# Kernel optimization log

Hardware: AMD Instinct MI355X
Metric: run time of the kernel (lower is better)

## Reference

```python
import jax, jax.numpy as jnp
import numpy as np

EPS = 1e-5

def _layernorm(x, g, b):
    # normalize over last (channel) axis
    mu = jnp.mean(x, axis=-1, keepdims=True)
    var = jnp.var(x, axis=-1, keepdims=True)
    return (x - mu) * jax.lax.rsqrt(var + EPS) * g + b

def _dynamix(xt, wnd, bnd, wnn, bnn):
    # xt: [B, M, N, C]; mixes over the N axis (vectorized form of the per-slice loop)
    B, M, N, C = xt.shape
    d = wnd.shape[1]
    p = xt @ wnd + bnd                       # [B,M,N,d]
    p = p.reshape(B, M, N * d) @ wnn + bnn   # [B,M,N*N]
    p = jax.nn.softmax(p.reshape(B, M, N, N), axis=-1)
    return jnp.einsum('bmij,bmjc->bmic', p, xt)  # [B,M,N,C]

def setup_inputs() -> dict:
    key = jax.random.key(0)
    ks = jax.random.split(key, 10)
    B, C, H, W, d, E = 32, 128, 56, 56, 10, 4
    def n(k, shape, scale=0.02):
        return jax.random.normal(k, shape, jnp.float32) * scale
    return {
        'x': jax.random.normal(ks[0], (B, C, H, W), jnp.float32),
        'ln1_g': jnp.ones((C,), jnp.float32), 'ln1_b': jnp.zeros((C,), jnp.float32),
        'h_wnd': n(ks[1], (C, d)), 'h_bnd': jnp.zeros((d,), jnp.float32),
        'h_wnn': n(ks[2], (W * d, W * W)), 'h_bnn': jnp.zeros((W * W,), jnp.float32),
        'w_wnd': n(ks[3], (C, d)), 'w_bnd': jnp.zeros((d,), jnp.float32),
        'w_wnn': n(ks[4], (H * d, H * H)), 'w_bnn': jnp.zeros((H * H,), jnp.float32),
        'pc_w': n(ks[5], (C, C)), 'pc_b': jnp.zeros((C,), jnp.float32),
        'po_w': n(ks[6], (C, C)), 'po_b': jnp.zeros((C,), jnp.float32),
        'ln2_g': jnp.ones((C,), jnp.float32), 'ln2_b': jnp.zeros((C,), jnp.float32),
        'fc1_w': n(ks[7], (C, E * C)), 'fc1_b': jnp.zeros((E * C,), jnp.float32),
        'fc2_w': n(ks[8], (E * C, C)), 'fc2_b': jnp.zeros((C,), jnp.float32),
    }

def reference(x, ln1_g, ln1_b, h_wnd, h_bnd, h_wnn, h_bnn,
              w_wnd, w_bnd, w_wnn, w_bnn, pc_w, pc_b, po_w, po_b,
              ln2_g, ln2_b, fc1_w, fc1_b, fc2_w, fc2_b):
    # x: [B,C,H,W] -> work channels-last [B,H,W,C]
    xt = jnp.transpose(x, (0, 2, 3, 1))
    # ---- block p1: LN + DynaMixer ----
    u = _layernorm(xt, ln1_g, ln1_b)                 # [B,H,W,C]
    y_h = _dynamix(u, h_wnd, h_bnd, h_wnn, h_bnn)    # mix over W per row
    u_w = jnp.transpose(u, (0, 2, 1, 3))             # [B,W,H,C]
    y_w = _dynamix(u_w, w_wnd, w_bnd, w_wnn, w_bnn)  # mix over H per col
    y_w = jnp.transpose(y_w, (0, 2, 1, 3))           # back to [B,H,W,C]
    y_c = u @ pc_w + pc_b                            # 1x1 conv proj_c
    y = (y_h + y_w + y_c) @ po_w + po_b              # 1x1 conv proj_o
    xt = xt + y                                      # residual (drop_path=0)
    # ---- block p2: LN + MLP ----
    v = _layernorm(xt, ln2_g, ln2_b)
    h = jax.nn.gelu(v @ fc1_w + fc1_b, approximate=False)
    h = h @ fc2_w + fc2_b
    xt = xt + h
    return jnp.transpose(xt, (0, 3, 1, 2))           # [B,C,H,W]
```

## Files before the change

### kernel.cpp

```cpp
#include <hip/hip_runtime.h>
#include <hip/hip_bf16.h>
#include <math.h>

#define BB 32
#define CC 128
#define HH 56
#define WW 56
#define HWHW 3136
#define TOK 100352
#define BH 1792
#define NDP 576
#define NNP 3200

typedef __attribute__((ext_vector_type(8))) short bhalf8;
typedef __attribute__((ext_vector_type(4))) float f32x4;
typedef __attribute__((ext_vector_type(4))) unsigned int u32x4;

__device__ inline unsigned short f2bf(float f) {
  __bf16 h = (__bf16)f;
  unsigned short u;
  __builtin_memcpy(&u, &h, 2);
  return u;
}
__device__ inline float bf2f(unsigned short u) {
  return __uint_as_float(((unsigned int)u) << 16);
}
__device__ inline unsigned int pack2(float a, float b) {
  return (unsigned int)f2bf(a) | ((unsigned int)f2bf(b) << 16);
}
__device__ inline f32x4 MFMA(bhalf8 a, bhalf8 b, f32x4 c) {
  return __builtin_amdgcn_mfma_f32_16x16x32_bf16(a, b, c, 0, 0, 0);
}
template <int CH>
__device__ inline bhalf8 ldsFrag(const unsigned short* base, int row, int chunk) {
  return *reinterpret_cast<const bhalf8*>(base + row * (CH * 8) + ((chunk ^ (row & 7)) * 8));
}
__device__ inline bhalf8 gFrag(const unsigned short* p) {
  return *reinterpret_cast<const bhalf8*>(p);
}
__device__ inline float gelu_f(float x) {
  float x3 = x * x * x;
  float z2 = 1.5957691216057308f * (x + 0.044715f * x3);
  float e = __expf(z2);
  return x * e * __builtin_amdgcn_rcpf(e + 1.0f);
}

__global__ __launch_bounds__(256) void wtrans_kernel(
    const float* __restrict__ hwnn, const float* __restrict__ wwnn,
    const float* __restrict__ pcw, const float* __restrict__ pow_,
    const float* __restrict__ fc1w, const float* __restrict__ fc2w,
    const float* __restrict__ hwnd, const float* __restrict__ wwnd,
    unsigned short* __restrict__ wnnTh, unsigned short* __restrict__ wnnTw,
    unsigned short* __restrict__ pcT, unsigned short* __restrict__ poT,
    unsigned short* __restrict__ fc1T, unsigned short* __restrict__ fc2T,
    unsigned short* __restrict__ wcatT, u32x4* __restrict__ pdzero) {
  __shared__ unsigned short t[64][65];
  int bid = blockIdx.x;
  int tid = threadIdx.x;
  if (bid >= 940) {
    int gt = (bid - 940) * 256 + tid, gs = 64 * 256;
    for (int i = gt; i < 258048; i += gs) { u32x4 z = {0, 0, 0, 0}; pdzero[i] = z; }
    for (int i = gt; i < 128 * 32; i += gs) {
      int k = i >> 5, n = i & 31;
      float v = n < 10 ? hwnd[k * 10 + n] : (n < 20 ? wwnd[k * 10 + (n - 10)] : 0.f);
      wcatT[n * 128 + k] = f2bf(v);
    }
    return;
  }
  const float* src; unsigned short* dst;
  int K, N, Kp, Np, bx, by;
  if (bid < 450)      { src = hwnn; dst = wnnTh; K = 560; N = 3136; Kp = 576; Np = 3200; int b = bid;       bx = b % 50; by = b / 50; }
  else if (bid < 900) { src = wwnn; dst = wnnTw; K = 560; N = 3136; Kp = 576; Np = 3200; int b = bid - 450; bx = b % 50; by = b / 50; }
  else if (bid < 904) { src = pcw;  dst = pcT;   K = 128; N = 128;  Kp = 128; Np = 128;  int b = bid - 900; bx = b % 2;  by = b / 2; }
  else if (bid < 908) { src = pow_; dst = poT;   K = 128; N = 128;  Kp = 128; Np = 128;  int b = bid - 904; bx = b % 2;  by = b / 2; }
  else if (bid < 924) { src = fc1w; dst = fc1T;  K = 128; N = 512;  Kp = 128; Np = 512;  int b = bid - 908; bx = b % 8;  by = b / 8; }
  else                { src = fc2w; dst = fc2T;  K = 512; N = 128;  Kp = 512; Np = 128;  int b = bid - 924; bx = b % 2;  by = b / 2; }
  int n0 = bx * 64, k0 = by * 64;
  for (int idx = tid; idx < 4096; idx += 256) {
    int kk = idx >> 6, nn = idx & 63;
    float v = (k0 + kk < K && n0 + nn < N) ? src[(size_t)(k0 + kk) * N + n0 + nn] : 0.f;
    t[nn][kk] = f2bf(v);
  }
  __syncthreads();
  for (int idx = tid; idx < 4096; idx += 256) {
    int nn = idx >> 6, kk = idx & 63;
    if (n0 + nn < Np && k0 + kk < Kp)
      dst[(size_t)(n0 + nn) * Kp + k0 + kk] = t[nn][kk];
  }
}

__global__ __launch_bounds__(256) void ln1_kernel(const float* __restrict__ x,
    const float* __restrict__ g, const float* __restrict__ bt,
    unsigned short* __restrict__ ubf, unsigned short* __restrict__ xcl) {
  int bh = blockIdx.x;
  int b = bh / HH, h = bh % HH;
  __shared__ float lds[WW][CC + 1];
  __shared__ float mu[WW], rs[WW];
  const float* xp = x + ((size_t)b * CC) * HWHW + (size_t)h * WW;
  for (int idx = threadIdx.x; idx < CC * WW; idx += 256) {
    int c = idx / WW, w = idx % WW;
    lds[w][c] = xp[(size_t)c * HWHW + w];
  }
  __syncthreads();
  if (threadIdx.x < WW) {
    int w = threadIdx.x;
    float s = 0.f, ss = 0.f;
    for (int c = 0; c < CC; ++c) { float v = lds[w][c]; s += v; ss += v * v; }
    float m = s * (1.0f / CC);
    float var = ss * (1.0f / CC) - m * m;
    mu[w] = m; rs[w] = rsqrtf(var + 1e-5f);
  }
  __syncthreads();
  unsigned short* up = ubf + (size_t)bh * (WW * CC);
  unsigned short* xc = xcl + (size_t)bh * (WW * CC);
  for (int idx = threadIdx.x; idx < WW * CC; idx += 256) {
    int w = idx >> 7, c = idx & 127;
    float v = lds[w][c];
    up[idx] = f2bf((v - mu[w]) * rs[w] * g[c] + bt[c]);
    xc[idx] = f2bf(v);
  }
}

__global__ __launch_bounds__(256) void pd_mfma(const unsigned short* __restrict__ ubf,
    const unsigned short* __restrict__ wcatT, const float* __restrict__ hbnd,
    const float* __restrict__ wbnd, unsigned short* __restrict__ pdh,
    unsigned short* __restrict__ pdw) {
  __shared__ __align__(16) unsigned short sU[64 * 128];
  __shared__ __align__(16) unsigned short sW[32 * 128];
  int tid = threadIdx.x;
  int tok0 = blockIdx.x * 64;
  #pragma unroll
  for (int i = 0; i < 4; ++i) {
    int s = i * 256 + tid; int r = s >> 4, c = s & 15;
    u32x4 v = *reinterpret_cast<const u32x4*>(ubf + (size_t)(tok0 + r) * 128 + c * 8);
    *reinterpret_cast<u32x4*>(sU + r * 128 + ((c ^ (r & 7)) * 8)) = v;
  }
  #pragma unroll
  for (int i = 0; i < 2; ++i) {
    int s = i * 256 + tid; int r = s >> 4, c = s & 15;
    u32x4 v = *reinterpret_cast<const u32x4*>(wcatT + (size_t)r * 128 + c * 8);
    *reinterpret_cast<u32x4*>(sW + r * 128 + ((c ^ (r & 7)) * 8)) = v;
  }
  __syncthreads();
  int wid = tid >> 6, lane = tid & 63, l16 = lane & 15, lk = lane >> 4;
  f32x4 acc[2] = {};
  #pragma unroll
  for (int kk = 0; kk < 4; ++kk) {
    bhalf8 a = ldsFrag<16>(sU, wid * 16 + l16, kk * 4 + lk);
    #pragma unroll
    for (int f = 0; f < 2; ++f) {
      bhalf8 b = ldsFrag<16>(sW, f * 16 + l16, kk * 4 + lk);
      acc[f] = MFMA(a, b, acc[f]);
    }
  }
  #pragma unroll
  for (int f = 0; f < 2; ++f) {
    int n = f * 16 + l16;
    #pragma unroll
    for (int r = 0; r < 4; ++r) {
      int tok = tok0 + wid * 16 + lk * 4 + r;
      float v = acc[f][r];
      if (n < 10) {
        pdh[((size_t)(tok / 56)) * NDP + (size_t)(tok % 56) * 10 + n] = f2bf(v + hbnd[n]);
      } else if (n < 20) {
        int b = tok / HWHW; int rem = tok % HWHW; int hh = rem / 56; int w = rem % 56;
        pdw[((size_t)(b * 56 + w)) * NDP + (size_t)hh * 10 + (n - 10)] = f2bf(v + wbnd[n - 10]);
      }
    }
  }
}

__global__ __launch_bounds__(256) void gemm_logits(
    const unsigned short* __restrict__ pdh, const unsigned short* __restrict__ pdw,
    const unsigned short* __restrict__ wnnTh, const unsigned short* __restrict__ wnnTw,
    const float* __restrict__ hbnn, const float* __restrict__ wbnn,
    unsigned short* __restrict__ ph, unsigned short* __restrict__ pwb) {
  __shared__ __align__(16) unsigned short sA[128 * 64];
  __shared__ __align__(16) unsigned short sB[128 * 64];
  int tid = threadIdx.x;
  int byr = blockIdx.y;
  const unsigned short* A; const unsigned short* BT; const float* bias; unsigned short* Cout;
  int row0;
  if (byr < 14) { A = pdh; BT = wnnTh; bias = hbnn; Cout = ph;  row0 = byr * 128; }
  else          { A = pdw; BT = wnnTw; bias = wbnn; Cout = pwb; row0 = (byr - 14) * 128; }
  int col0 = blockIdx.x * 128;
  int wid = tid >> 6, lane = tid & 63;
  int wm = wid >> 1, wn = wid & 1;
  int l16 = lane & 15, lk = lane >> 4;
  f32x4 acc[4][4] = {};
  for (int k0 = 0; k0 < NDP; k0 += 64) {
    #pragma unroll
    for (int i = 0; i < 4; ++i) {
      int s = i * 256 + tid; int r = s >> 3, c = s & 7;
      u32x4 v = *reinterpret_cast<const u32x4*>(A + (size_t)(row0 + r) * NDP + k0 + c * 8);
      *reinterpret_cast<u32x4*>(sA + r * 64 + ((c ^ (r & 7)) * 8)) = v;
    }
    #pragma unroll
    for (int i = 0; i < 4; ++i) {
      int s = i * 256 + tid; int r = s >> 3, c = s & 7;
      u32x4 v = *reinterpret_cast<const u32x4*>(BT + (size_t)(col0 + r) * NDP + k0 + c * 8);
      *reinterpret_cast<u32x4*>(sB + r * 64 + ((c ^ (r & 7)) * 8)) = v;
    }
    __syncthreads();
    bhalf8 af[4][2], bf[4][2];
    #pragma unroll
    for (int f = 0; f < 4; ++f)
      #pragma unroll
      for (int kk = 0; kk < 2; ++kk) {
        af[f][kk] = ldsFrag<8>(sA, wm * 64 + f * 16 + l16, kk * 4 + lk);
        bf[f][kk] = ldsFrag<8>(sB, wn * 64 + f * 16 + l16, kk * 4 + lk);
      }
    #pragma unroll
    for (int i = 0; i < 4; ++i)
      #pragma unroll
      for (int j = 0; j < 4; ++j) {
        acc[i][j] = MFMA(af[i][0], bf[j][0], acc[i][j]);
        acc[i][j] = MFMA(af[i][1], bf[j][1], acc[i][j]);
      }
    __syncthreads();
  }
  #pragma unroll
  for (int i = 0; i < 4; ++i) {
    int rbase = row0 + wm * 64 + i * 16 + lk * 4;
    #pragma unroll
    for (int j = 0; j < 4; ++j) {
      int col = col0 + wn * 64 + j * 16 + l16;
      if (col < HWHW) {
        float bv = bias[col];
        #pragma unroll
        for (int r = 0; r < 4; ++r)
          Cout[(size_t)(rbase + r) * NNP + col] = f2bf(acc[i][j][r] + bv);
      }
    }
  }
}

__global__ __launch_bounds__(256) void softmax56_kernel(unsigned short* __restrict__ ph,
                                                        unsigned short* __restrict__ pw) {
  int wave = (blockIdx.x * 256 + threadIdx.x) >> 6;
  int lane = threadIdx.x & 63;
  if (wave >= 2 * TOK) return;
  unsigned short* buf = wave < TOK ? ph : pw;
  int row = wave < TOK ? wave : wave - TOK;
  int bh = row / 56, i = row % 56;
  unsigned short* p = buf + (size_t)bh * NNP + (size_t)i * 56;
  float xv = lane < WW ? bf2f(p[lane]) : -INFINITY;
  float m = xv;
  for (int o = 32; o > 0; o >>= 1) m = fmaxf(m, __shfl_xor(m, o));
  float e = lane < WW ? __expf(xv - m) : 0.f;
  float s = e;
  for (int o = 32; o > 0; o >>= 1) s += __shfl_xor(s, o);
  if (lane < WW) p[lane] = f2bf(e * __builtin_amdgcn_rcpf(s));
}

__global__ __launch_bounds__(256) void mixh_pc(const unsigned short* __restrict__ ph,
    const unsigned short* __restrict__ ubf, const unsigned short* __restrict__ pcT,
    const float* __restrict__ pcb, unsigned short* __restrict__ accm) {
  int bh = blockIdx.x;
  int tok0 = bh * 56;
  __shared__ __align__(16) unsigned short sUt[128 * 64];
  int tid = threadIdx.x;
  for (int s = tid; s < 1024; s += 256) {
    int j = s >> 4, cc = s & 15;
    unsigned short e8[8] = {0, 0, 0, 0, 0, 0, 0, 0};
    if (j < 56)
      *reinterpret_cast<u32x4*>(e8) =
          *reinterpret_cast<const u32x4*>(ubf + (size_t)(tok0 + j) * 128 + cc * 8);
    #pragma unroll
    for (int e = 0; e < 8; ++e) {
      int cf = cc * 8 + e;
      sUt[cf * 64 + (((j >> 3) ^ (cf & 7)) * 8) + (j & 7)] = e8[e];
    }
  }
  __syncthreads();
  int lane = tid & 63, l16 = lane & 15, lk = lane >> 4, wn = tid >> 6;
  const unsigned short* prow = ph + (size_t)bh * NNP;
  f32x4 acc[4][2] = {};
  #pragma unroll
  for (int kk = 0; kk < 2; ++kk) {
    bhalf8 a[4], b[2];
    #pragma unroll
    for (int i = 0; i < 4; ++i)
      a[i] = gFrag(prow + (i * 16 + l16) * 56 + (kk * 4 + lk) * 8);
    #pragma unroll
    for (int j = 0; j < 2; ++j) b[j] = ldsFrag<8>(sUt, wn * 32 + j * 16 + l16, kk * 4 + lk);
    #pragma unroll
    for (int i = 0; i < 4; ++i)
      #pragma unroll
      for (int j = 0; j < 2; ++j) acc[i][j] = MFMA(a[i], b[j], acc[i][j]);
  }
  #pragma unroll
  for (int kk = 0; kk < 4; ++kk) {
    bhalf8 a[4], b[2];
    #pragma unroll
    for (int i = 0; i < 4; ++i)
      a[i] = gFrag(ubf + (size_t)(tok0 + i * 16 + l16) * 128 + (kk * 4 + lk) * 8);
    #pragma unroll
    for (int j = 0; j < 2; ++j)
      b[j] = gFrag(pcT + (size_t)(wn * 32 + j * 16 + l16) * 128 + (kk * 4 + lk) * 8);
    #pragma unroll
    for (int i = 0; i < 4; ++i)
      #pragma unroll
      for (int j = 0; j < 2; ++j) acc[i][j] = MFMA(a[i], b[j], acc[i][j]);
  }
  #pragma unroll
  for (int i = 0; i < 4; ++i) {
    int tok = i * 16 + lk * 4;
    #pragma unroll
    for (int j = 0; j < 2; ++j) {
      int c = wn * 32 + j * 16 + l16;
      float bv = pcb[c];
      #pragma unroll
      for (int r = 0; r < 4; ++r)
        if (tok + r < 56)
          accm[(size_t)(tok0 + tok + r) * 128 + c] = f2bf(acc[i][j][r] + bv);
    }
  }
}

__global__ __launch_bounds__(256) void mixw_fin(const unsigned short* __restrict__ pw,
    const unsigned short* __restrict__ ubf, const unsigned short* __restrict__ poT,
    const float* __restrict__ pob, const unsigned short* __restrict__ xcl,
    unsigned short* __restrict__ accXt,
    const float* __restrict__ ln2g, const float* __restrict__ ln2b,
    unsigned short* __restrict__ vbf) {
  int bw = blockIdx.x;
  int bq = bw / 56, w = bw % 56;
  __shared__ __align__(16) unsigned short sUt[128 * 64];
  __shared__ __align__(16) unsigned short sS[64 * 128];
  int tid = threadIdx.x;
  for (int s = tid; s < 1024; s += 256) {
    int j = s >> 4, cc = s & 15;
    unsigned short e8[8] = {0, 0, 0, 0, 0, 0, 0, 0};
    if (j < 56)
      *reinterpret_cast<u32x4*>(e8) =
          *reinterpret_cast<const u32x4*>(ubf + ((size_t)bq * HWHW + (size_t)j * 56 + w) * 128 + cc * 8);
    #pragma unroll
    for (int e = 0; e < 8; ++e) {
      int cf = cc * 8 + e;
      sUt[cf * 64 + (((j >> 3) ^ (cf & 7)) * 8) + (j & 7)] = e8[e];
    }
  }
  for (int s = tid; s < 1024; s += 256) {
    int r = s >> 4, c = s & 15;
    u32x4 v = {0, 0, 0, 0};
    if (r < 56) v = *reinterpret_cast<const u32x4*>(accXt + ((size_t)bq * HWHW + (size_t)r * 56 + w) * 128 + c * 8);
    *reinterpret_cast<u32x4*>(sS + r * 128 + ((c ^ (r & 7)) * 8)) = v;
  }
  __syncthreads();
  int lane = tid & 63, l16 = lane & 15, lk = lane >> 4, wn = tid >> 6;
  const unsigned short* prow = pw + (size_t)bw * NNP;
  f32x4 acc1[4][2] = {};
  #pragma unroll
  for (int kk = 0; kk < 2; ++kk) {
    bhalf8 a[4], b[2];
    #pragma unroll
    for (int i = 0; i < 4; ++i)
      a[i] = gFrag(prow + (i * 16 + l16) * 56 + (kk * 4 + lk) * 8);
    #pragma unroll
    for (int j = 0; j < 2; ++j) b[j] = ldsFrag<8>(sUt, wn * 32 + j * 16 + l16, kk * 4 + lk);
    #pragma unroll
    for (int i = 0; i < 4; ++i)
      #pragma unroll
      for (int j = 0; j < 2; ++j) acc1[i][j] = MFMA(a[i], b[j], acc1[i][j]);
  }
  __syncthreads();
  #pragma unroll
  for (int i = 0; i < 4; ++i) {
    #pragma unroll
    for (int j = 0; j < 2; ++j) {
      int col = wn * 32 + j * 16 + l16;
      #pragma unroll
      for (int r = 0; r < 4; ++r) {
        int row = i * 16 + lk * 4 + r;
        int ad = row * 128 + (((col >> 3) ^ (row & 7)) * 8) + (col & 7);
        sS[ad] = f2bf(bf2f(sS[ad]) + acc1[i][j][r]);
      }
    }
  }
  __syncthreads();
  f32x4 acc2[4][2] = {};
  #pragma unroll
  for (int kk = 0; kk < 4; ++kk) {
    bhalf8 a[4], b[2];
    #pragma unroll
    for (int i = 0; i < 4; ++i) a[i] = ldsFrag<16>(sS, i * 16 + l16, kk * 4 + lk);
    #pragma unroll
    for (int j = 0; j < 2; ++j)
      b[j] = gFrag(poT + (size_t)(wn * 32 + j * 16 + l16) * 128 + (kk * 4 + lk) * 8);
    #pragma unroll
    for (int i = 0; i < 4; ++i)
      #pragma unroll
      for (int j = 0; j < 2; ++j) acc2[i][j] = MFMA(a[i], b[j], acc2[i][j]);
  }
  __syncthreads();
  #pragma unroll
  for (int i = 0; i < 4; ++i) {
    #pragma unroll
    for (int j = 0; j < 2; ++j) {
      int c = wn * 32 + j * 16 + l16;
      float bv = pob[c];
      #pragma unroll
      for (int r = 0; r < 4; ++r) {
        int row = i * 16 + lk * 4 + r;
        if (row < 56) {
          size_t t = (size_t)bq * HWHW + (size_t)row * 56 + w;
          float z = acc2[i][j][r] + bv + bf2f(xcl[t * 128 + c]);
          unsigned short zb = f2bf(z);
          accXt[t * 128 + c] = zb;
          sS[row * 128 + (((c >> 3) ^ (row & 7)) * 8) + (c & 7)] = zb;
        }
      }
    }
  }
  __syncthreads();
  {
    int wid4 = tid >> 6;
    int c0 = 2 * lane;
    float g0 = ln2g[c0], g1 = ln2g[c0 + 1];
    float b0 = ln2b[c0], b1 = ln2b[c0 + 1];
    for (int row = wid4; row < 56; row += 4) {
      int ad = row * 128 + (((c0 >> 3) ^ (row & 7)) * 8) + (c0 & 7);
      unsigned int wrd = *reinterpret_cast<const unsigned int*>(sS + ad);
      float z0 = bf2f((unsigned short)(wrd & 0xFFFFu));
      float z1 = bf2f((unsigned short)(wrd >> 16));
      float s1 = z0 + z1, s2 = z0 * z0 + z1 * z1;
      for (int o = 32; o > 0; o >>= 1) { s1 += __shfl_xor(s1, o); s2 += __shfl_xor(s2, o); }
      float m = s1 * (1.0f / CC);
      float var = s2 * (1.0f / CC) - m * m;
      float rv = rsqrtf(var + 1e-5f);
      float n0 = (z0 - m) * rv * g0 + b0;
      float n1 = (z1 - m) * rv * g1 + b1;
      size_t t = (size_t)bq * HWHW + (size_t)row * 56 + w;
      *reinterpret_cast<unsigned int*>(vbf + t * 128 + c0) = pack2(n0, n1);
    }
  }
}

__global__ __launch_bounds__(256) void gemm_fc1(const unsigned short* __restrict__ vbf,
    const unsigned short* __restrict__ fc1T, const float* __restrict__ b1,
    unsigned short* __restrict__ hbuf) {
  __shared__ __align__(16) unsigned short sW[128 * 64];
  __shared__ __align__(16) unsigned short sV[128 * 64];
  __shared__ float b1s[128];
  int tid = threadIdx.x;
  int id = blockIdx.x;
  int xcd = id & 7, sub = id >> 3;
  int tok0 = (xcd * 98 + (sub >> 2)) * 128;
  int hidT = (sub & 3) * 128;
  if (tid < 128) b1s[tid] = b1[hidT + tid];
  int wid = tid >> 6, lane = tid & 63;
  int wm = wid >> 1, wn = wid & 1;
  int l16 = lane & 15, lk = lane >> 4;
  f32x4 acc[4][4] = {};
  for (int k0 = 0; k0 < 128; k0 += 64) {
    #pragma unroll
    for (int i = 0; i < 4; ++i) {
      int s = i * 256 + tid; int r = s >> 3, c = s & 7;
      u32x4 v = *reinterpret_cast<const u32x4*>(fc1T + (size_t)(hidT + r) * 128 + k0 + c * 8);
      *reinterpret_cast<u32x4*>(sW + r * 64 + ((c ^ (r & 7)) * 8)) = v;
    }
    #pragma unroll
    for (int i = 0; i < 4; ++i) {
      int s = i * 256 + tid; int r = s >> 3, c = s & 7;
      u32x4 v = *reinterpret_cast<const u32x4*>(vbf + (size_t)(tok0 + r) * 128 + k0 + c * 8);
      *reinterpret_cast<u32x4*>(sV + r * 64 + ((c ^ (r & 7)) * 8)) = v;
    }
    __syncthreads();
    bhalf8 af[4][2], bf[4][2];
    #pragma unroll
    for (int f = 0; f < 4; ++f)
      #pragma unroll
      for (int kk = 0; kk < 2; ++kk) {
        af[f][kk] = ldsFrag<8>(sW, wm * 64 + f * 16 + l16, kk * 4 + lk);
        bf[f][kk] = ldsFrag<8>(sV, wn * 64 + f * 16 + l16, kk * 4 + lk);
      }
    #pragma unroll
    for (int i = 0; i < 4; ++i)
      #pragma unroll
      for (int j = 0; j < 4; ++j) {
        acc[i][j] = MFMA(af[i][0], bf[j][0], acc[i][j]);
        acc[i][j] = MFMA(af[i][1], bf[j][1], acc[i][j]);
      }
    __syncthreads();
  }
  #pragma unroll
  for (int i = 0; i < 4; ++i) {
    int hidL = wm * 64 + i * 16 + lk * 4;
    #pragma unroll
    for (int j = 0; j < 4; ++j) {
      int tokL = wn * 64 + j * 16 + l16;
      float v0 = gelu_f(acc[i][j][0] + b1s[hidL]);
      float v1 = gelu_f(acc[i][j][1] + b1s[hidL + 1]);
      float v2 = gelu_f(acc[i][j][2] + b1s[hidL + 2]);
      float v3 = gelu_f(acc[i][j][3] + b1s[hidL + 3]);
      unsigned long long pk = (unsigned long long)pack2(v0, v1)
                            | ((unsigned long long)pack2(v2, v3) << 32);
      *reinterpret_cast<unsigned long long*>(
          hbuf + (size_t)(tok0 + tokL) * 512 + hidT + hidL) = pk;
    }
  }
}

__global__ __launch_bounds__(256) void gemm_fc2(const unsigned short* __restrict__ hbuf,
    const unsigned short* __restrict__ fc2T, const float* __restrict__ b2,
    const unsigned short* __restrict__ xt2, float* __restrict__ out) {
  __shared__ __align__(16) unsigned short smem[2][128 * 64];
  __shared__ float b2s[128];
  unsigned short* sH = smem[0];
  unsigned short* sC = smem[1];
  unsigned short* xtile = &smem[0][0];
  int tid = threadIdx.x;
  int tok0 = blockIdx.x * 128;
  if (tid < 128) b2s[tid] = b2[tid];
  int wid = tid >> 6, lane = tid & 63;
  int wm = wid >> 1, wn = wid & 1;
  int l16 = lane & 15, lk = lane >> 4;
  f32x4 acc[4][4] = {};
  for (int k0 = 0; k0 < 512; k0 += 64) {
    #pragma unroll
    for (int i = 0; i < 4; ++i) {
      int s = i * 256 + tid; int r = s >> 3, c = s & 7;
      u32x4 v = *reinterpret_cast<const u32x4*>(hbuf + (size_t)(tok0 + r) * 512 + k0 + c * 8);
      *reinterpret_cast<u32x4*>(sH + r * 64 + ((c ^ (r & 7)) * 8)) = v;
    }
    #pragma unroll
    for (int i = 0; i < 4; ++i) {
      int s = i * 256 + tid; int r = s >> 3, c = s & 7;
      u32x4 v = *reinterpret_cast<const u32x4*>(fc2T + (size_t)r * 512 + k0 + c * 8);
      *reinterpret_cast<u32x4*>(sC + r * 64 + ((c ^ (r & 7)) * 8)) = v;
    }
    __syncthreads();
    bhalf8 af[4][2], bf[4][2];
    #pragma unroll
    for (int f = 0; f < 4; ++f)
      #pragma unroll
      for (int kk = 0; kk < 2; ++kk) {
        af[f][kk] = ldsFrag<8>(sH, wm * 64 + f * 16 + l16, kk * 4 + lk);
        bf[f][kk] = ldsFrag<8>(sC, wn * 64 + f * 16 + l16, kk * 4 + lk);
      }
    #pragma unroll
    for (int i = 0; i < 4; ++i)
      #pragma unroll
      for (int j = 0; j < 4; ++j) {
        acc[i][j] = MFMA(af[i][0], bf[j][0], acc[i][j]);
        acc[i][j] = MFMA(af[i][1], bf[j][1], acc[i][j]);
      }
    __syncthreads();
  }
  #pragma unroll
  for (int i = 0; i < 8; ++i) {
    int s = i * 256 + tid; int r = s >> 4, c = s & 15;
    u32x4 v = *reinterpret_cast<const u32x4*>(xt2 + (size_t)(tok0 + r) * 128 + c * 8);
    *reinterpret_cast<u32x4*>(xtile + r * 128 + c * 8) = v;
  }
  __syncthreads();
  #pragma unroll
  for (int i = 0; i < 4; ++i) {
    int tokL = wm * 64 + i * 16 + lk * 4;
    int tokG = tok0 + tokL;
    int bqv = tokG / HWHW;
    int pos = tokG - bqv * HWHW;
    #pragma unroll
    for (int j = 0; j < 4; ++j) {
      int cL = wn * 64 + j * 16 + l16;
      float bv = b2s[cL];
      f32x4 o;
      #pragma unroll
      for (int r = 0; r < 4; ++r)
        o[r] = acc[i][j][r] + bv + bf2f(xtile[(tokL + r) * 128 + cL]);
      *reinterpret_cast<f32x4*>(out + ((size_t)(bqv * CC + cL)) * HWHW + pos) = o;
    }
  }
}

extern "C" void kernel_launch(void* const* d_in, const int* in_sizes, int n_in,
                              void* d_out, int out_size, void* d_ws, size_t ws_size,
                              hipStream_t stream) {
  const float* x     = (const float*)d_in[0];
  const float* ln1_g = (const float*)d_in[1];
  const float* ln1_b = (const float*)d_in[2];
  const float* h_wnd = (const float*)d_in[3];
  const float* h_bnd = (const float*)d_in[4];
  const float* h_wnn = (const float*)d_in[5];
  const float* h_bnn = (const float*)d_in[6];
  const float* w_wnd = (const float*)d_in[7];
  const float* w_bnd = (const float*)d_in[8];
  const float* w_wnn = (const float*)d_in[9];
  const float* w_bnn = (const float*)d_in[10];
  const float* pc_w  = (const float*)d_in[11];
  const float* pc_b  = (const float*)d_in[12];
  const float* po_w  = (const float*)d_in[13];
  const float* po_b  = (const float*)d_in[14];
  const float* ln2_g = (const float*)d_in[15];
  const float* ln2_b = (const float*)d_in[16];
  const float* fc1_w = (const float*)d_in[17];
  const float* fc1_b = (const float*)d_in[18];
  const float* fc2_w = (const float*)d_in[19];
  const float* fc2_b = (const float*)d_in[20];
  float* out = (float*)d_out;
  char* ws = (char*)d_ws;

  unsigned short* ubf   = (unsigned short*)(ws + 0);
  unsigned short* xcl   = (unsigned short*)(ws + 25690112);
  unsigned short* accXt = (unsigned short*)(ws + 51380224);
  unsigned short* pdh   = (unsigned short*)(ws + 77070336);
  unsigned short* pdw   = (unsigned short*)(ws + 79134720);
  unsigned short* ph    = (unsigned short*)(ws + 81199104);
  unsigned short* pw    = (unsigned short*)(ws + 92667904);
  unsigned short* wnnTh = (unsigned short*)(ws + 104136704);
  unsigned short* wnnTw = (unsigned short*)(ws + 107823104);
  unsigned short* hbuf  = (unsigned short*)(ws + 77070336);
  unsigned short* pcT   = (unsigned short*)(ws + 179830784);
  unsigned short* poT   = (unsigned short*)(ws + 179863552);
  unsigned short* fc1T  = (unsigned short*)(ws + 179896320);
  unsigned short* fc2T  = (unsigned short*)(ws + 180027392);
  unsigned short* wcatT = (unsigned short*)(ws + 180158464);
  unsigned short* vbf   = ubf;

  wtrans_kernel<<<1004, 256, 0, stream>>>(h_wnn, w_wnn, pc_w, po_w, fc1_w, fc2_w,
      h_wnd, w_wnd, wnnTh, wnnTw, pcT, poT, fc1T, fc2T, wcatT, (u32x4*)pdh);
  ln1_kernel<<<BH, 256, 0, stream>>>(x, ln1_g, ln1_b, ubf, xcl);
  pd_mfma<<<TOK / 64, 256, 0, stream>>>(ubf, wcatT, h_bnd, w_bnd, pdh, pdw);
  gemm_logits<<<dim3(NNP / 128, 28), 256, 0, stream>>>(pdh, pdw, wnnTh, wnnTw,
      h_bnn, w_bnn, ph, pw);
  softmax56_kernel<<<(2 * TOK) / 4, 256, 0, stream>>>(ph, pw);
  mixh_pc<<<BH, 256, 0, stream>>>(ph, ubf, pcT, pc_b, accXt);
  mixw_fin<<<BB * WW, 256, 0, stream>>>(pw, ubf, poT, po_b, xcl, accXt,
      ln2_g, ln2_b, vbf);
  gemm_fc1<<<3136, 256, 0, stream>>>(vbf, fc1T, fc1_b, hbuf);
  gemm_fc2<<<TOK / 128, 256, 0, stream>>>(hbuf, fc2T, fc2_b, accXt, out);
}
```

Baseline: 268.7 us.

## Store transposed (W-major) copies so column-mix kernel reads contiguous slabs

The LN1 kernel now writes an extra W-major transposed copy of the normalized activations and writes the residual input in transposed layout. mixh_pc writes its output in that same transposed layout. mixw_fin can then load each column as one contiguous 56x128 slab instead of doing strided per-token gathers, and it stages the residual tile in shared memory. This trades an extra 25 MB write in LN1, scattered strided writes in LN1 and mixh_pc, and more LDS per block for coalesced reads in mixw_fin.

```diff
diff --git a/kernel.cpp b/kernel.cpp
--- a/kernel.cpp
+++ b/kernel.cpp
@@ -91,7 +91,8 @@
 
 __global__ __launch_bounds__(256) void ln1_kernel(const float* __restrict__ x,
     const float* __restrict__ g, const float* __restrict__ bt,
-    unsigned short* __restrict__ ubf, unsigned short* __restrict__ xcl) {
+    unsigned short* __restrict__ ubf, unsigned short* __restrict__ ubfT,
+    unsigned short* __restrict__ xcl) {
   int bh = blockIdx.x;
   int b = bh / HH, h = bh % HH;
   __shared__ float lds[WW][CC + 1];
@@ -112,12 +113,16 @@
   }
   __syncthreads();
   unsigned short* up = ubf + (size_t)bh * (WW * CC);
-  unsigned short* xc = xcl + (size_t)bh * (WW * CC);
+  size_t tbase = ((size_t)b * HWHW + h) * 128;
   for (int idx = threadIdx.x; idx < WW * CC; idx += 256) {
     int w = idx >> 7, c = idx & 127;
     float v = lds[w][c];
-    up[idx] = f2bf((v - mu[w]) * rs[w] * g[c] + bt[c]);
-    xc[idx] = f2bf(v);
+    float uv = (v - mu[w]) * rs[w] * g[c] + bt[c];
+    unsigned short ub = f2bf(uv);
+    up[idx] = ub;
+    size_t ta = tbase + (size_t)w * (56 * 128) + c;
+    ubfT[ta] = ub;
+    xcl[ta] = f2bf(v);
   }
 }
 
@@ -255,8 +260,9 @@
 
 __global__ __launch_bounds__(256) void mixh_pc(const unsigned short* __restrict__ ph,
     const unsigned short* __restrict__ ubf, const unsigned short* __restrict__ pcT,
-    const float* __restrict__ pcb, unsigned short* __restrict__ accm) {
+    const float* __restrict__ pcb, unsigned short* __restrict__ accmT) {
   int bh = blockIdx.x;
+  int b = bh / HH, h = bh % HH;
   int tok0 = bh * 56;
   __shared__ __align__(16) unsigned short sUt[128 * 64];
   int tid = threadIdx.x;
@@ -313,28 +319,33 @@
       #pragma unroll
       for (int r = 0; r < 4; ++r)
         if (tok + r < 56)
-          accm[(size_t)(tok0 + tok + r) * 128 + c] = f2bf(acc[i][j][r] + bv);
+          accmT[((size_t)b * HWHW + (size_t)(tok + r) * 56 + h) * 128 + c] =
+              f2bf(acc[i][j][r] + bv);
     }
   }
 }
 
 __global__ __launch_bounds__(256) void mixw_fin(const unsigned short* __restrict__ pw,
-    const unsigned short* __restrict__ ubf, const unsigned short* __restrict__ poT,
-    const float* __restrict__ pob, const unsigned short* __restrict__ xcl,
-    unsigned short* __restrict__ accXt,
+    const unsigned short* __restrict__ ubfT, const unsigned short* __restrict__ poT,
+    const float* __restrict__ pob, const unsigned short* __restrict__ xclT,
+    const unsigned short* __restrict__ accmT, unsigned short* __restrict__ accXt,
     const float* __restrict__ ln2g, const float* __restrict__ ln2b,
     unsigned short* __restrict__ vbf) {
   int bw = blockIdx.x;
   int bq = bw / 56, w = bw % 56;
   __shared__ __align__(16) unsigned short sUt[128 * 64];
   __shared__ __align__(16) unsigned short sS[64 * 128];
+  __shared__ __align__(16) unsigned short xtile[56 * 128];
   int tid = threadIdx.x;
+  size_t slab = ((size_t)bq * HWHW + (size_t)w * 56) * 128;
+  const unsigned short* uslab = ubfT + slab;
+  const unsigned short* aslab = accmT + slab;
+  const unsigned short* xslab = xclT + slab;
   for (int s = tid; s < 1024; s += 256) {
     int j = s >> 4, cc = s & 15;
     unsigned short e8[8] = {0, 0, 0, 0, 0, 0, 0, 0};
     if (j < 56)
-      *reinterpret_cast<u32x4*>(e8) =
-          *reinterpret_cast<const u32x4*>(ubf + ((size_t)bq * HWHW + (size_t)j * 56 + w) * 128 + cc * 8);
+      *reinterpret_cast<u32x4*>(e8) = *reinterpret_cast<const u32x4*>(uslab + j * 128 + cc * 8);
     #pragma unroll
     for (int e = 0; e < 8; ++e) {
       int cf = cc * 8 + e;
@@ -344,9 +355,11 @@
   for (int s = tid; s < 1024; s += 256) {
     int r = s >> 4, c = s & 15;
     u32x4 v = {0, 0, 0, 0};
-    if (r < 56) v = *reinterpret_cast<const u32x4*>(accXt + ((size_t)bq * HWHW + (size_t)r * 56 + w) * 128 + c * 8);
+    if (r < 56) v = *reinterpret_cast<const u32x4*>(aslab + r * 128 + c * 8);
     *reinterpret_cast<u32x4*>(sS + r * 128 + ((c ^ (r & 7)) * 8)) = v;
   }
+  for (int s = tid; s < 896; s += 256)
+    *reinterpret_cast<u32x4*>(xtile + s * 8) = *reinterpret_cast<const u32x4*>(xslab + s * 8);
   __syncthreads();
   int lane = tid & 63, l16 = lane & 15, lk = lane >> 4, wn = tid >> 6;
   const unsigned short* prow = pw + (size_t)bw * NNP;
@@ -405,7 +418,7 @@
         int row = i * 16 + lk * 4 + r;
         if (row < 56) {
           size_t t = (size_t)bq * HWHW + (size_t)row * 56 + w;
-          float z = acc2[i][j][r] + bv + bf2f(xcl[t * 128 + c]);
+          float z = acc2[i][j][r] + bv + bf2f(xtile[row * 128 + c]);
           unsigned short zb = f2bf(z);
           accXt[t * 128 + c] = zb;
           sS[row * 128 + (((c >> 3) ^ (row & 7)) * 8) + (c & 7)] = zb;
@@ -602,7 +615,7 @@
   char* ws = (char*)d_ws;
 
   unsigned short* ubf   = (unsigned short*)(ws + 0);
-  unsigned short* xcl   = (unsigned short*)(ws + 25690112);
+  unsigned short* xclT  = (unsigned short*)(ws + 25690112);
   unsigned short* accXt = (unsigned short*)(ws + 51380224);
   unsigned short* pdh   = (unsigned short*)(ws + 77070336);
   unsigned short* pdw   = (unsigned short*)(ws + 79134720);
@@ -616,17 +629,19 @@
   unsigned short* fc1T  = (unsigned short*)(ws + 179896320);
   unsigned short* fc2T  = (unsigned short*)(ws + 180027392);
   unsigned short* wcatT = (unsigned short*)(ws + 180158464);
+  unsigned short* ubfT  = (unsigned short*)(ws + 180166656);
+  unsigned short* accmT = (unsigned short*)(ws + 205856768);
   unsigned short* vbf   = ubf;
 
   wtrans_kernel<<<1004, 256, 0, stream>>>(h_wnn, w_wnn, pc_w, po_w, fc1_w, fc2_w,
       h_wnd, w_wnd, wnnTh, wnnTw, pcT, poT, fc1T, fc2T, wcatT, (u32x4*)pdh);
-  ln1_kernel<<<BH, 256, 0, stream>>>(x, ln1_g, ln1_b, ubf, xcl);
+  ln1_kernel<<<BH, 256, 0, stream>>>(x, ln1_g, ln1_b, ubf, ubfT, xclT);
   pd_mfma<<<TOK / 64, 256, 0, stream>>>(ubf, wcatT, h_bnd, w_bnd, pdh, pdw);
   gemm_logits<<<dim3(NNP / 128, 28), 256, 0, stream>>>(pdh, pdw, wnnTh, wnnTw,
       h_bnn, w_bnn, ph, pw);
   softmax56_kernel<<<(2 * TOK) / 4, 256, 0, stream>>>(ph, pw);
-  mixh_pc<<<BH, 256, 0, stream>>>(ph, ubf, pcT, pc_b, accXt);
-  mixw_fin<<<BB * WW, 256, 0, stream>>>(pw, ubf, poT, po_b, xcl, accXt,
+  mixh_pc<<<BH, 256, 0, stream>>>(ph, ubf, pcT, pc_b, accmT);
+  mixw_fin<<<BB * WW, 256, 0, stream>>>(pw, ubfT, poT, po_b, xclT, accmT, accXt,
       ln2_g, ln2_b, vbf);
   gemm_fc1<<<3136, 256, 0, stream>>>(vbf, fc1T, fc1_b, hbuf);
   gemm_fc2<<<TOK / 128, 256, 0, stream>>>(hbuf, fc2T, fc2_b, accXt, out);
```

Result: slower. 281.0 us (+4.6%).
